# Kernel tuning notes

Measured on AMD Instinct MI355X. Metric: run time of the kernel, lower is better.

## Reference

```python
import jax, jax.numpy as jnp
import numpy as np

T, H2, G = 32768, 4096, 8   # tokens, x last dim, num groups
H = H2 // 2                  # output last dim
INT_SCALE, CLIP_MIN, CLIP_MAX = 127.0, -128.0, 127.0  # int8


def setup_inputs() -> dict:
    key = jax.random.key(0)
    k1, k2, k3 = jax.random.split(key, 3)
    x = jax.random.normal(k1, (T, H2), dtype=jnp.float32)
    smooth_scales = jax.random.uniform(k2, (G, H), dtype=jnp.float32, minval=0.5, maxval=1.5)
    group_index = jnp.sort(jax.random.randint(k3, (G,), 0, T, dtype=jnp.int32))  # cumsum-style ends
    return {"x": x, "smooth_scales": smooth_scales, "group_index": group_index,
            "quant_mode": 1, "group_list_type": 0}


def reference(x, smooth_scales, group_index, quant_mode, group_list_type):
    # SwiGLU (activate_left=False): silu(right) * left
    xf = x.astype(jnp.float32)
    x_left, x_right = xf[..., :H], xf[..., H:]
    out = x_left * (jax.nn.sigmoid(x_right) * x_right)  # [T, H]

    # Group boundaries: cumsum mode -> group i covers rows [ends[i-1], ends[i])
    ends = group_index if group_list_type == 0 else jnp.cumsum(group_index)
    rows = jnp.arange(out.shape[0])
    gid = jnp.searchsorted(ends, rows, side='right')  # [T], == G for rows past last end
    valid = gid < G                                    # rows past last boundary stay unscaled
    s = smooth_scales[jnp.clip(gid, 0, G - 1)]         # [T, H]
    scaled = jnp.where(valid[:, None], out * s, out)

    # Dynamic per-row quantization (quant_mode == 1)
    y_max = jnp.maximum(jnp.max(jnp.abs(scaled), axis=-1, keepdims=True), 1e-10)
    dyn_scale = INT_SCALE / y_max                      # [T, 1]
    q = jnp.round(jnp.clip(scaled * dyn_scale, CLIP_MIN, CLIP_MAX)).astype(jnp.int8)
    return q, dyn_scale[:, 0]
```

## Files before the change

kernel.cpp:

```cpp
#include <hip/hip_runtime.h>
#include <math.h>

constexpr int T_  = 32768;
constexpr int H_  = 2048;
constexpr int H2_ = 4096;
constexpr int G_  = 8;

__global__ __launch_bounds__(256) void swiglu_quant_kernel(
    const float* __restrict__ x,
    const float* __restrict__ smooth,
    const int*   __restrict__ group_idx,
    const int*   __restrict__ glt_ptr,
    float* __restrict__ q_out,
    float* __restrict__ scale_out)
{
    const int row = blockIdx.x;
    const int tid = threadIdx.x;

    const int glt = glt_ptr[0];
    int gid = 0;
    int acc = 0;
    #pragma unroll
    for (int g = 0; g < G_; ++g) {
        const int v = group_idx[g];
        int e;
        if (glt == 0) { e = v; } else { acc += v; e = acc; }
        gid += (e <= row) ? 1 : 0;
    }
    const bool valid = (gid < G_);
    const int sg = valid ? gid : (G_ - 1);
    const float* __restrict__ srow = smooth + (size_t)sg * H_;

    const float4* __restrict__ xl4 = reinterpret_cast<const float4*>(x + (size_t)row * H2_);
    const float4* __restrict__ xr4 = reinterpret_cast<const float4*>(x + (size_t)row * H2_ + H_);
    const float4* __restrict__ s4  = reinterpret_cast<const float4*>(srow);

    float vals[8];
    float amax = 0.0f;

    #pragma unroll
    for (int i = 0; i < 2; ++i) {
        const int idx4 = tid + i * 256;
        const float4 l = xl4[idx4];
        const float4 r = xr4[idx4];
        float4 s;
        if (valid) s = s4[idx4];
        else       s = make_float4(1.0f, 1.0f, 1.0f, 1.0f);

        float o;
        o = l.x * (r.x / (1.0f + expf(-r.x))); o *= s.x; vals[i*4+0] = o; amax = fmaxf(amax, fabsf(o));
        o = l.y * (r.y / (1.0f + expf(-r.y))); o *= s.y; vals[i*4+1] = o; amax = fmaxf(amax, fabsf(o));
        o = l.z * (r.z / (1.0f + expf(-r.z))); o *= s.z; vals[i*4+2] = o; amax = fmaxf(amax, fabsf(o));
        o = l.w * (r.w / (1.0f + expf(-r.w))); o *= s.w; vals[i*4+3] = o; amax = fmaxf(amax, fabsf(o));
    }

    #pragma unroll
    for (int off = 32; off > 0; off >>= 1)
        amax = fmaxf(amax, __shfl_xor(amax, off, 64));

    __shared__ float wmax[4];
    const int wid  = tid >> 6;
    if ((tid & 63) == 0) wmax[wid] = amax;
    __syncthreads();
    float m = fmaxf(fmaxf(wmax[0], wmax[1]), fmaxf(wmax[2], wmax[3]));
    m = fmaxf(m, 1e-10f);
    const float dyn = 127.0f / m;

    float4* __restrict__ q4 = reinterpret_cast<float4*>(q_out + (size_t)row * H_);
    #pragma unroll
    for (int i = 0; i < 2; ++i) {
        const int idx4 = tid + i * 256;
        float4 o;
        o.x = rintf(fminf(fmaxf(vals[i*4+0] * dyn, -128.0f), 127.0f));
        o.y = rintf(fminf(fmaxf(vals[i*4+1] * dyn, -128.0f), 127.0f));
        o.z = rintf(fminf(fmaxf(vals[i*4+2] * dyn, -128.0f), 127.0f));
        o.w = rintf(fminf(fmaxf(vals[i*4+3] * dyn, -128.0f), 127.0f));
        q4[idx4] = o;
    }

    if (tid == 0) scale_out[row] = dyn;
}

extern "C" void kernel_launch(void* const* d_in, const int* in_sizes, int n_in,
                              void* d_out, int out_size, void* d_ws, size_t ws_size,
                              hipStream_t stream) {
    const float* x      = (const float*)d_in[0];
    const float* smooth = (const float*)d_in[1];
    const int*   gidx   = (const int*)d_in[2];
    const int*   glt    = (const int*)d_in[4];

    float* q_out     = (float*)d_out;
    float* scale_out = (float*)d_out + (size_t)T_ * H_;

    swiglu_quant_kernel<<<T_, 256, 0, stream>>>(x, smooth, gidx, glt, q_out, scale_out);
}
```

Measured before the change: 746.5 us.

## Map one row per wavefront and use nontemporal loads/stores

Each 64-lane wavefront now processes a whole row, with four rows per block, so the row max reduction uses only wave shuffles and no shared memory or block barrier. Every lane holds 32 elements per row in registers, loaded as batched vector loads of the left, right and scale halves. The streaming x loads and q stores are marked nontemporal to reduce cache pollution. Register pressure rises and there are fewer waves per element, which may reduce latency hiding on a memory-bound kernel.

```diff
diff --git a/kernel.cpp b/kernel.cpp
--- a/kernel.cpp
+++ b/kernel.cpp
@@ -6,7 +6,9 @@
 constexpr int H2_ = 4096;
 constexpr int G_  = 8;
 
-__global__ __launch_bounds__(256) void swiglu_quant_kernel(
+typedef float fx4 __attribute__((ext_vector_type(4)));
+
+__global__ __launch_bounds__(256) void swiglu_quant_wave(
     const float* __restrict__ x,
     const float* __restrict__ smooth,
     const int*   __restrict__ group_idx,
@@ -14,8 +16,9 @@
     float* __restrict__ q_out,
     float* __restrict__ scale_out)
 {
-    const int row = blockIdx.x;
-    const int tid = threadIdx.x;
+    const int wid  = threadIdx.x >> 6;
+    const int lane = threadIdx.x & 63;
+    const int row  = (blockIdx.x << 2) | wid;
 
     const int glt = glt_ptr[0];
     int gid = 0;
@@ -28,57 +31,58 @@
         gid += (e <= row) ? 1 : 0;
     }
     const bool valid = (gid < G_);
-    const int sg = valid ? gid : (G_ - 1);
-    const float* __restrict__ srow = smooth + (size_t)sg * H_;
+    const float* __restrict__ srow = smooth + (size_t)(valid ? gid : (G_ - 1)) * H_;
 
-    const float4* __restrict__ xl4 = reinterpret_cast<const float4*>(x + (size_t)row * H2_);
-    const float4* __restrict__ xr4 = reinterpret_cast<const float4*>(x + (size_t)row * H2_ + H_);
-    const float4* __restrict__ s4  = reinterpret_cast<const float4*>(srow);
+    const fx4* __restrict__ xl4 = reinterpret_cast<const fx4*>(x + (size_t)row * H2_);
+    const fx4* __restrict__ xr4 = xl4 + (H_ / 4);
+    const fx4* __restrict__ s4  = reinterpret_cast<const fx4*>(srow);
 
-    float vals[8];
-    float amax = 0.0f;
+    fx4 v[8];
+    fx4 r[8];
+    fx4 s[8];
 
     #pragma unroll
-    for (int i = 0; i < 2; ++i) {
-        const int idx4 = tid + i * 256;
-        const float4 l = xl4[idx4];
-        const float4 r = xr4[idx4];
-        float4 s;
-        if (valid) s = s4[idx4];
-        else       s = make_float4(1.0f, 1.0f, 1.0f, 1.0f);
+    for (int i = 0; i < 8; ++i) v[i] = __builtin_nontemporal_load(&xl4[lane + 64 * i]);
+    #pragma unroll
+    for (int i = 0; i < 8; ++i) r[i] = __builtin_nontemporal_load(&xr4[lane + 64 * i]);
+    if (valid) {
+        #pragma unroll
+        for (int i = 0; i < 8; ++i) s[i] = s4[lane + 64 * i];
+    } else {
+        #pragma unroll
+        for (int i = 0; i < 8; ++i) s[i] = (fx4){1.0f, 1.0f, 1.0f, 1.0f};
+    }
 
-        float o;
-        o = l.x * (r.x / (1.0f + expf(-r.x))); o *= s.x; vals[i*4+0] = o; amax = fmaxf(amax, fabsf(o));
-        o = l.y * (r.y / (1.0f + expf(-r.y))); o *= s.y; vals[i*4+1] = o; amax = fmaxf(amax, fabsf(o));
-        o = l.z * (r.z / (1.0f + expf(-r.z))); o *= s.z; vals[i*4+2] = o; amax = fmaxf(amax, fabsf(o));
-        o = l.w * (r.w / (1.0f + expf(-r.w))); o *= s.w; vals[i*4+3] = o; amax = fmaxf(amax, fabsf(o));
+    float amax = 0.0f;
+    #pragma unroll
+    for (int i = 0; i < 8; ++i) {
+        #pragma unroll
+        for (int j = 0; j < 4; ++j) {
+            const float xr = r[i][j];
+            const float o = v[i][j] * (xr / (1.0f + expf(-xr))) * s[i][j];
+            v[i][j] = o;
+            amax = fmaxf(amax, fabsf(o));
+        }
     }
 
     #pragma unroll
     for (int off = 32; off > 0; off >>= 1)
         amax = fmaxf(amax, __shfl_xor(amax, off, 64));
 
-    __shared__ float wmax[4];
-    const int wid  = tid >> 6;
-    if ((tid & 63) == 0) wmax[wid] = amax;
-    __syncthreads();
-    float m = fmaxf(fmaxf(wmax[0], wmax[1]), fmaxf(wmax[2], wmax[3]));
-    m = fmaxf(m, 1e-10f);
+    const float m   = fmaxf(amax, 1e-10f);
     const float dyn = 127.0f / m;
 
-    float4* __restrict__ q4 = reinterpret_cast<float4*>(q_out + (size_t)row * H_);
+    fx4* __restrict__ q4 = reinterpret_cast<fx4*>(q_out + (size_t)row * H_);
     #pragma unroll
-    for (int i = 0; i < 2; ++i) {
-        const int idx4 = tid + i * 256;
-        float4 o;
-        o.x = rintf(fminf(fmaxf(vals[i*4+0] * dyn, -128.0f), 127.0f));
-        o.y = rintf(fminf(fmaxf(vals[i*4+1] * dyn, -128.0f), 127.0f));
-        o.z = rintf(fminf(fmaxf(vals[i*4+2] * dyn, -128.0f), 127.0f));
-        o.w = rintf(fminf(fmaxf(vals[i*4+3] * dyn, -128.0f), 127.0f));
-        q4[idx4] = o;
+    for (int i = 0; i < 8; ++i) {
+        fx4 o;
+        #pragma unroll
+        for (int j = 0; j < 4; ++j)
+            o[j] = rintf(fminf(fmaxf(v[i][j] * dyn, -128.0f), 127.0f));
+        __builtin_nontemporal_store(o, &q4[lane + 64 * i]);
     }
 
-    if (tid == 0) scale_out[row] = dyn;
+    if (lane == 0) scale_out[row] = dyn;
 }
 
 extern "C" void kernel_launch(void* const* d_in, const int* in_sizes, int n_in,
@@ -92,5 +96,5 @@
     float* q_out     = (float*)d_out;
     float* scale_out = (float*)d_out + (size_t)T_ * H_;
 
-    swiglu_quant_kernel<<<T_, 256, 0, stream>>>(x, smooth, gidx, glt, q_out, scale_out);
+    swiglu_quant_wave<<<T_ / 4, 256, 0, stream>>>(x, smooth, gidx, glt, q_out, scale_out);
 }
```

After: 734.0 us. Within noise of the previous version (-1.7%).
